# Kernel optimization log

Measured on AMD Instinct MI355X. Metric: run time of the kernel, lower is better.

Reference implementation:

```python
import jax, jax.numpy as jnp
import numpy as np


def setup_inputs() -> dict:
    key = jax.random.key(0)
    k1, k2, k3 = jax.random.split(key, 3)
    bs, r, d = 4, 4096, 64
    G = jax.random.uniform(k1, (bs, d), dtype=jnp.float32)          # eigenvalues (non-negative)
    V = jax.random.normal(k2, (bs, r, d), dtype=jnp.float32)        # eigenvectors / spectral embedding
    weights = jax.random.uniform(k3, (1,), dtype=jnp.float32)       # learned scalar t
    return {"G": G, "V": V, "weights": weights}


def reference(G, V, weights):
    # Original: eVs = diag(max(G,0)^(2t)); y = E@eVs@Phi2^T + Phi2@eVs@E^T - 2*Phi@eVs@Phi^T
    # Since eVs is diagonal, this is the weighted pairwise squared distance:
    # y[b,i,j] = sum_k w[b,k] * (V[b,i,k] - V[b,j,k])^2 with w = max(G,0)^(2t).
    t = weights[0]
    w = jnp.maximum(G, jnp.zeros_like(G)) ** (2.0 * t)   # (bs, d)
    Vw = V * w[:, None, :]                               # (bs, r, d) elementwise diag scaling
    s = jnp.sum(Vw * V, axis=-1)                         # (bs, r): weighted squared norms
    cross = jnp.einsum('brd,bsd->brs', Vw, V)            # (bs, r, r)
    y = s[:, :, None] + s[:, None, :] - 2.0 * cross
    return y
```

## Files before the change

kernel.cpp:

```cpp
#include <hip/hip_runtime.h>
#include <hip/hip_bf16.h>


typedef __attribute__((ext_vector_type(8))) short bf16x8;
typedef __attribute__((ext_vector_type(4))) float f32x4;

constexpr int BS = 4, R = 4096, D = 64;
constexpr int LS = 260;

__global__ __launch_bounds__(256) void prep_kernel(
    const float* __restrict__ G, const float* __restrict__ V,
    const float* __restrict__ wt,
    __hip_bfloat16* __restrict__ vw_bf, __hip_bfloat16* __restrict__ v_bf,
    float* __restrict__ s)
{
    int row  = blockIdx.x * 4 + (threadIdx.x >> 6);
    int lane = threadIdx.x & 63;
    if (row >= BS * R) return;
    int b = row / R;

    float t2 = 2.0f * wt[0];
    float g  = fmaxf(G[b * D + lane], 0.0f);
    float w  = powf(g, t2);
    float v  = V[(size_t)row * D + lane];

    __hip_bfloat16 vb  = __float2bfloat16(v);
    __hip_bfloat16 vwb = __float2bfloat16(w * v);
    v_bf [(size_t)row * D + lane] = vb;
    vw_bf[(size_t)row * D + lane] = vwb;

    float prod = __bfloat162float(vwb) * __bfloat162float(vb);
    #pragma unroll
    for (int off = 32; off; off >>= 1) prod += __shfl_down(prod, off);
    if (lane == 0) s[row] = prod;
}

__global__ __launch_bounds__(256) void dist_kernel(
    const short* __restrict__ vw_bf, const short* __restrict__ v_bf,
    const float* __restrict__ s, float* __restrict__ out)
{
    __shared__ float lds[32 * LS];

    int lane = threadIdx.x & 63;
    int wave = threadIdx.x >> 6;
    int b  = blockIdx.z;
    int i0 = blockIdx.y * 32;
    int jb = blockIdx.x * 256;
    int j0 = jb + wave * 64;

    const short* A  = vw_bf + ((size_t)b * R + i0) * D;
    const short* B  = v_bf  + ((size_t)b * R + j0) * D;
    const float* sb = s + (size_t)b * R;

    int lrow = lane & 15;
    int kgrp = lane >> 4;

    bf16x8 a[2][2];
    #pragma unroll
    for (int rb = 0; rb < 2; ++rb)
        #pragma unroll
        for (int ks = 0; ks < 2; ++ks)
            a[rb][ks] = *(const bf16x8*)(A + (rb * 16 + lrow) * D + ks * 32 + kgrp * 8);

    f32x4 acc[2][4];
    #pragma unroll
    for (int rb = 0; rb < 2; ++rb)
        #pragma unroll
        for (int jt = 0; jt < 4; ++jt)
            acc[rb][jt] = f32x4{0.f, 0.f, 0.f, 0.f};

    #pragma unroll
    for (int jt = 0; jt < 4; ++jt) {
        const short* Bt = B + jt * 16 * D;
        bf16x8 b0 = *(const bf16x8*)(Bt + lrow * D +      kgrp * 8);
        bf16x8 b1 = *(const bf16x8*)(Bt + lrow * D + 32 + kgrp * 8);
        #pragma unroll
        for (int rb = 0; rb < 2; ++rb) {
            acc[rb][jt] = __builtin_amdgcn_mfma_f32_16x16x32_bf16(a[rb][0], b0, acc[rb][jt], 0, 0, 0);
            acc[rb][jt] = __builtin_amdgcn_mfma_f32_16x16x32_bf16(a[rb][1], b1, acc[rb][jt], 0, 0, 0);
        }
    }

    float si_lane = sb[i0 + (lane & 31)];
    #pragma unroll
    for (int rb = 0; rb < 2; ++rb) {
        #pragma unroll
        for (int rg = 0; rg < 4; ++rg) {
            int row  = rb * 16 + kgrp * 4 + rg;
            float si = __shfl(si_lane, row);
            #pragma unroll
            for (int jt = 0; jt < 4; ++jt) {
                float sj = sb[j0 + jt * 16 + lrow];
                float y  = si + sj - 2.0f * acc[rb][jt][rg];
                lds[row * LS + wave * 64 + jt * 16 + lrow] = y;
            }
        }
    }

    __syncthreads();

    float* outb = out + ((size_t)b * R + i0) * R + jb;
    #pragma unroll
    for (int r = 0; r < 8; ++r) {
        int row = wave * 8 + r;
        f32x4 v = *(const f32x4*)&lds[row * LS + lane * 4];
        *(f32x4*)(outb + (size_t)row * R + lane * 4) = v;
    }
}

extern "C" void kernel_launch(void* const* d_in, const int* in_sizes, int n_in,
                              void* d_out, int out_size, void* d_ws, size_t ws_size,
                              hipStream_t stream) {
    const float* G  = (const float*)d_in[0];
    const float* V  = (const float*)d_in[1];
    const float* wt = (const float*)d_in[2];
    float* out = (float*)d_out;

    char* ws = (char*)d_ws;
    __hip_bfloat16* vw_bf = (__hip_bfloat16*)ws;
    __hip_bfloat16* v_bf  = (__hip_bfloat16*)(ws + (size_t)BS * R * D * 2);
    float*          s     = (float*)        (ws + (size_t)BS * R * D * 4);

    prep_kernel<<<BS * R / 4, 256, 0, stream>>>(G, V, wt, vw_bf, v_bf, s);

    dim3 grid(R / 256, R / 32, BS);
    dist_kernel<<<grid, 256, 0, stream>>>((const short*)vw_bf, (const short*)v_bf,
                                          s, out);
}
```

Before: 72.38 us.

## Enlarge dist tile to 128x256 with 8 waves, staged LDS output, nontemporal stores

```diff
diff --git a/kernel.cpp b/kernel.cpp
--- a/kernel.cpp
+++ b/kernel.cpp
@@ -35,36 +35,38 @@
     if (lane == 0) s[row] = prod;
 }
 
-__global__ __launch_bounds__(256) void dist_kernel(
+__global__ __launch_bounds__(512) void dist_kernel(
     const short* __restrict__ vw_bf, const short* __restrict__ v_bf,
     const float* __restrict__ s, float* __restrict__ out)
 {
-    __shared__ float lds[32 * LS];
+    __shared__ float lds[64 * LS];
 
     int lane = threadIdx.x & 63;
     int wave = threadIdx.x >> 6;
+    int wr   = wave >> 2;
+    int wc   = wave & 3;
+
     int b  = blockIdx.z;
-    int i0 = blockIdx.y * 32;
     int jb = blockIdx.x * 256;
-    int j0 = jb + wave * 64;
+    int i0 = blockIdx.y * 128;
 
-    const short* A  = vw_bf + ((size_t)b * R + i0) * D;
-    const short* B  = v_bf  + ((size_t)b * R + j0) * D;
+    const short* A  = vw_bf + ((size_t)b * R + i0 + wr * 64) * D;
+    const short* B  = v_bf  + ((size_t)b * R + jb + wc * 64) * D;
     const float* sb = s + (size_t)b * R;
 
     int lrow = lane & 15;
     int kgrp = lane >> 4;
 
-    bf16x8 a[2][2];
+    bf16x8 a[4][2];
     #pragma unroll
-    for (int rb = 0; rb < 2; ++rb)
+    for (int rb = 0; rb < 4; ++rb)
         #pragma unroll
         for (int ks = 0; ks < 2; ++ks)
             a[rb][ks] = *(const bf16x8*)(A + (rb * 16 + lrow) * D + ks * 32 + kgrp * 8);
 
-    f32x4 acc[2][4];
+    f32x4 acc[4][4];
     #pragma unroll
-    for (int rb = 0; rb < 2; ++rb)
+    for (int rb = 0; rb < 4; ++rb)
         #pragma unroll
         for (int jt = 0; jt < 4; ++jt)
             acc[rb][jt] = f32x4{0.f, 0.f, 0.f, 0.f};
@@ -75,36 +77,44 @@
         bf16x8 b0 = *(const bf16x8*)(Bt + lrow * D +      kgrp * 8);
         bf16x8 b1 = *(const bf16x8*)(Bt + lrow * D + 32 + kgrp * 8);
         #pragma unroll
-        for (int rb = 0; rb < 2; ++rb) {
+        for (int rb = 0; rb < 4; ++rb) {
             acc[rb][jt] = __builtin_amdgcn_mfma_f32_16x16x32_bf16(a[rb][0], b0, acc[rb][jt], 0, 0, 0);
             acc[rb][jt] = __builtin_amdgcn_mfma_f32_16x16x32_bf16(a[rb][1], b1, acc[rb][jt], 0, 0, 0);
         }
     }
 
-    float si_lane = sb[i0 + (lane & 31)];
+    float si_lane = sb[i0 + wr * 64 + lane];
+
+    float* outb = out + ((size_t)b * R + i0) * R + jb;
+
     #pragma unroll
-    for (int rb = 0; rb < 2; ++rb) {
-        #pragma unroll
-        for (int rg = 0; rg < 4; ++rg) {
-            int row  = rb * 16 + kgrp * 4 + rg;
-            float si = __shfl(si_lane, row);
+    for (int c = 0; c < 2; ++c) {
+        if (wr == c) {
             #pragma unroll
-            for (int jt = 0; jt < 4; ++jt) {
-                float sj = sb[j0 + jt * 16 + lrow];
-                float y  = si + sj - 2.0f * acc[rb][jt][rg];
-                lds[row * LS + wave * 64 + jt * 16 + lrow] = y;
+            for (int rb = 0; rb < 4; ++rb) {
+                #pragma unroll
+                for (int rg = 0; rg < 4; ++rg) {
+                    int rl = rb * 16 + kgrp * 4 + rg;
+                    float si = __shfl(si_lane, rl);
+                    #pragma unroll
+                    for (int jt = 0; jt < 4; ++jt) {
+                        float sj = sb[jb + wc * 64 + jt * 16 + lrow];
+                        float y  = si + sj - 2.0f * acc[rb][jt][rg];
+                        lds[rl * LS + wc * 64 + jt * 16 + lrow] = y;
+                    }
+                }
             }
         }
-    }
+        __syncthreads();
 
-    __syncthreads();
-
-    float* outb = out + ((size_t)b * R + i0) * R + jb;
-    #pragma unroll
-    for (int r = 0; r < 8; ++r) {
-        int row = wave * 8 + r;
-        f32x4 v = *(const f32x4*)&lds[row * LS + lane * 4];
-        *(f32x4*)(outb + (size_t)row * R + lane * 4) = v;
+        #pragma unroll
+        for (int r = 0; r < 8; ++r) {
+            int rl = wave * 8 + r;
+            f32x4 v = *(const f32x4*)&lds[rl * LS + lane * 4];
+            __builtin_nontemporal_store(v,
+                (f32x4*)(outb + (size_t)(c * 64 + rl) * R + lane * 4));
+        }
+        if (c == 0) __syncthreads();
     }
 }
 
@@ -123,7 +133,7 @@
 
     prep_kernel<<<BS * R / 4, 256, 0, stream>>>(G, V, wt, vw_bf, v_bf, s);
 
-    dim3 grid(R / 256, R / 32, BS);
-    dist_kernel<<<grid, 256, 0, stream>>>((const short*)vw_bf, (const short*)v_bf,
+    dim3 grid(R / 256, R / 128, BS);
+    dist_kernel<<<grid, 512, 0, stream>>>((const short*)vw_bf, (const short*)v_bf,
                                           s, out);
 }
```

New measurement: 66.72 us. -7.8%, faster.
